# Kernel optimization log

Hardware: AMD Instinct MI355X
Metric: run time of the kernel (lower is better)

## Reference

```python
import jax, jax.numpy as jnp
import numpy as np

B, S, D = 32, 2048, 8
H = 256
COUPLING = -1.0  # TC['WOBBLE_COUPLING'] default
WOBBLE_STEP = 0.03125


def setup_inputs() -> dict:
    key = jax.random.key(0)
    k = jax.random.split(key, 5)
    return {
        'x': jax.random.normal(k[0], (B, S, D), dtype=jnp.float32),
        'We': jax.random.normal(k[1], (H, D), dtype=jnp.float32) * 0.35,
        'be': jax.random.normal(k[2], (H,), dtype=jnp.float32) * 0.02,
        'Wr': jax.random.normal(k[3], (256, 7 * H), dtype=jnp.float32) * 0.02,
        'br': jax.random.normal(k[4], (256,), dtype=jnp.float32) * 0.02,
    }


def _forward(x, We, be, Wr, br):
    Bm, Sm, _ = x.shape
    h = We.shape[0]

    def step(carry, xt):
        ph, wb, prev_xt, has_prev = carry
        pt = xt @ We.T + be                      # [B,h] embedded phase increments
        # xpt = stack([cos(pt), sin(pt)]); accumulator consumes the spinor pair,
        # equivalent to the wrapped phase delta atan2(sin, cos)
        delta = jnp.arctan2(jnp.sin(pt), jnp.cos(pt))
        wb2 = wb + WOBBLE_STEP
        is_rep = has_prev * jnp.all(xt == prev_xt, axis=1, keepdims=True).astype(x.dtype)
        # WobblePhaseAccumulator(spinor=True): phase advances by delta plus
        # coupling-modulated wobble; wobble channel accumulates delta
        ph_out = ph + delta + COUPLING * jnp.sin(wb2)
        wb_out = wb2 + delta
        ph_new = ph_out
        wb_new = is_rep * wb_out + (1.0 - is_rep) * wb2
        ph_s = 0.5 * ph_new
        readout = jnp.concatenate([
            jnp.cos(ph_new), jnp.sin(ph_new),
            jnp.cos(ph_s), jnp.sin(ph_s),
            jnp.cos(wb_new), jnp.sin(wb_new),
            ph_new,
        ], axis=1)                                # [B, 7h]
        logits = readout @ Wr.T + br              # [B, 256]
        return (ph_new, wb_new, xt, jnp.ones((), x.dtype)), (logits, ph_new, wb_new)

    ph0 = jnp.zeros((Bm, h), x.dtype)
    wb0 = jnp.zeros((Bm, h), x.dtype)
    prev0 = jnp.zeros((Bm, x.shape[2]), x.dtype)
    carry0 = (ph0, wb0, prev0, jnp.zeros((), x.dtype))
    xs = jnp.swapaxes(x, 0, 1)                    # [S,B,D]
    _, (logits, ph_hist, wb_hist) = jax.lax.scan(step, carry0, xs)
    logits = jnp.swapaxes(logits, 0, 1)           # [B,S,256]
    ph_hist = jnp.swapaxes(ph_hist, 0, 1)         # [B,S,h]
    wb_hist = jnp.swapaxes(wb_hist, 0, 1)         # [B,S,h]
    return logits, ph_hist, wb_hist


def reference(x, We, be, Wr, br):
    return _forward(x, We, be, Wr, br)
```

## Files before the change

kernel.cpp:

```cpp
#include <hip/hip_runtime.h>
#include <hip/hip_bf16.h>
#include <math.h>

#define NB 32
#define NS 2048
#define ND 8
#define NH 256
#define NK 1792
#define NO 256
#define NM (NB*NS)
#define WSTEP 0.03125f
#define CCH 64
#define LCH (NS/CCH)

typedef __attribute__((ext_vector_type(8))) short short8;
typedef __attribute__((ext_vector_type(4))) float f32x4;

__device__ float g_ssum[NB*CCH*NH];
__device__ float g_wb0 [NB*CCH*NH];
__device__ float g_esum[NB*CCH*NH];
__device__ float g_ph0 [NB*CCH*NH];
__device__ float g_rep [NB*NS];

__device__ __forceinline__ float fast_sin(float x){
    float r = x * 0.15915494309189535f;
    r = r - floorf(r);
    return __builtin_amdgcn_sinf(r);
}
__device__ __forceinline__ float fast_cos(float x){
    float r = x * 0.15915494309189535f;
    r = r - floorf(r);
    return __builtin_amdgcn_cosf(r);
}
__device__ __forceinline__ unsigned short bf16_rn(float f){
    union { float f; unsigned int u; } v; v.f = f;
    unsigned int u = v.u;
    unsigned int r = (u + 0x7FFFu + ((u >> 16) & 1u)) >> 16;
    return (unsigned short)r;
}
__device__ __forceinline__ float xform(int c, float v){
    switch(c){
        case 0: case 4: return fast_cos(v);
        case 1: case 5: return fast_sin(v);
        case 2:         return fast_cos(0.5f*v);
        case 3:         return fast_sin(0.5f*v);
        default:        return v;
    }
}

extern "C" __global__ __launch_bounds__(256)
void k_delta(const float* __restrict__ x, const float* __restrict__ We,
             const float* __restrict__ be, float* __restrict__ delta){
    int blk = blockIdx.x;
    int b = blk >> 6;
    int c = blk & (CCH-1);
    int t0 = c * LCH;
    int h = threadIdx.x;
    __shared__ float xs[(LCH+1)*ND];
    __shared__ float rep[LCH];

    for(int i = h; i < (LCH+1)*ND/4; i += 256){
        int row  = i >> 1;
        int col4 = (i & 1) * 4;
        int t = t0 - 1 + row; if(t < 0) t = 0;
        *(float4*)&xs[row*ND + col4] = *(const float4*)&x[((size_t)b*NS + t)*ND + col4];
    }
    __syncthreads();
    if(h < LCH){
        int t = t0 + h;
        float fl = 0.f;
        if(t > 0){
            bool eq = true;
            #pragma unroll
            for(int d2 = 0; d2 < ND; ++d2) eq = eq && (xs[(h+1)*ND+d2] == xs[h*ND+d2]);
            fl = eq ? 1.f : 0.f;
        }
        rep[h] = fl;
        g_rep[b*NS + t] = fl;
    }
    __syncthreads();

    float4 w0 = *(const float4*)&We[h*ND];
    float4 w1 = *(const float4*)&We[h*ND + 4];
    float bh = be[h];
    float ssum = 0.f;
    for(int j = 0; j < LCH; ++j){
        const float* xr = &xs[(j+1)*ND];
        float pt = bh + xr[0]*w0.x + xr[1]*w0.y + xr[2]*w0.z + xr[3]*w0.w
                      + xr[4]*w1.x + xr[5]*w1.y + xr[6]*w1.z + xr[7]*w1.w;
        float s, cc;
        sincosf(pt, &s, &cc);
        float d = atan2f(s, cc);
        delta[((size_t)(t0+j)*NB + b)*NH + h] = d;
        ssum += WSTEP + rep[j]*d;
    }
    g_ssum[(b*CCH + c)*NH + h] = ssum;
}

extern "C" __global__ __launch_bounds__(256)
void k_prefix_s(){
    int g = blockIdx.x*256 + threadIdx.x;
    int b = g >> 8, h = g & 255;
    float acc = 0.f;
    for(int c = 0; c < CCH; ++c){
        size_t idx = ((size_t)(b*CCH + c))*NH + h;
        g_wb0[idx] = acc;
        acc += g_ssum[idx];
    }
}
extern "C" __global__ __launch_bounds__(256)
void k_prefix_e(){
    int g = blockIdx.x*256 + threadIdx.x;
    int b = g >> 8, h = g & 255;
    float acc = 0.f;
    for(int c = 0; c < CCH; ++c){
        size_t idx = ((size_t)(b*CCH + c))*NH + h;
        g_ph0[idx] = acc;
        acc += g_esum[idx];
    }
}

extern "C" __global__ __launch_bounds__(256)
void k_escan(const float* __restrict__ delta, float* __restrict__ wb_hist){
    int blk = blockIdx.x;
    int b = blk >> 6, c = blk & (CCH-1), t0 = c*LCH, h = threadIdx.x;
    __shared__ float rep[LCH];
    if(h < LCH) rep[h] = g_rep[b*NS + t0 + h];
    __syncthreads();
    float wb = g_wb0[(b*CCH + c)*NH + h];
    const float* dp = delta + (size_t)t0*NB*NH + b*NH + h;
    float* wp = wb_hist + ((size_t)b*NS + t0)*NH + h;
    float d[LCH];
    #pragma unroll
    for(int j = 0; j < LCH; ++j) d[j] = dp[(size_t)j*(NB*NH)];
    float esum = 0.f;
    #pragma unroll
    for(int j = 0; j < LCH; ++j){
        float wb2 = wb + WSTEP;
        float e = d[j] - sinf(wb2);
        esum += e;
        wb = wb2 + rep[j]*d[j];
        wp[(size_t)j*NH] = wb;
    }
    g_esum[(b*CCH + c)*NH + h] = esum;
}

extern "C" __global__ __launch_bounds__(256)
void k_phw(const float* __restrict__ delta, float* __restrict__ ph_hist){
    int blk = blockIdx.x;
    int b = blk >> 6, c = blk & (CCH-1), t0 = c*LCH, h = threadIdx.x;
    __shared__ float rep[LCH];
    if(h < LCH) rep[h] = g_rep[b*NS + t0 + h];
    __syncthreads();
    float wb = g_wb0[(b*CCH + c)*NH + h];
    float ph = g_ph0[(b*CCH + c)*NH + h];
    const float* dp = delta + (size_t)t0*NB*NH + b*NH + h;
    float* pp = ph_hist + ((size_t)b*NS + t0)*NH + h;
    float d[LCH];
    #pragma unroll
    for(int j = 0; j < LCH; ++j) d[j] = dp[(size_t)j*(NB*NH)];
    #pragma unroll
    for(int j = 0; j < LCH; ++j){
        float wb2 = wb + WSTEP;
        float e = d[j] - sinf(wb2);
        ph += e;
        wb = wb2 + rep[j]*d[j];
        pp[(size_t)j*NH] = ph;
    }
}

extern "C" __global__ __launch_bounds__(512)
void k_logits(const float* __restrict__ ph_hist, const float* __restrict__ wb_hist,
              const float* __restrict__ Wr, const float* __restrict__ br,
              float* __restrict__ logits){
    __shared__ __align__(16) unsigned short Al[128][40];
    __shared__ __align__(16) unsigned short Bl[256][40];
    int tid  = threadIdx.x;
    int m0   = blockIdx.x * 128;
    int lane = tid & 63, wid = tid >> 6;
    int wm = wid >> 2, wn = wid & 3;

    f32x4 acc[4][4];
    f32x4 zz = {0.f, 0.f, 0.f, 0.f};
    #pragma unroll
    for(int i = 0; i < 4; ++i)
        #pragma unroll
        for(int j = 0; j < 4; ++j) acc[i][j] = zz;

    int arow = tid >> 2, ah = (tid & 3) * 8;
    int bn   = tid >> 1, bk = (tid & 1) * 16;

    for(int ks = 0; ks < NK/32; ++ks){
        int k0 = ks * 32;
        int c  = k0 >> 8;
        int hb = k0 & 255;

        {
            const float* src = (c == 4 || c == 5) ? wb_hist : ph_hist;
            const float* p = src + (size_t)(m0 + arow)*NH + hb + ah;
            float4 v0 = *(const float4*)p;
            float4 v1 = *(const float4*)(p + 4);
            float v[8] = {v0.x, v0.y, v0.z, v0.w, v1.x, v1.y, v1.z, v1.w};
            unsigned int pk[4];
            #pragma unroll
            for(int j = 0; j < 4; ++j){
                float a0 = xform(c, v[2*j]);
                float a1 = xform(c, v[2*j+1]);
                pk[j] = (unsigned int)bf16_rn(a0) | ((unsigned int)bf16_rn(a1) << 16);
            }
            *(uint4*)&Al[arow][ah] = make_uint4(pk[0], pk[1], pk[2], pk[3]);
        }
        {
            const float* q = Wr + (size_t)bn*NK + k0 + bk;
            float4 q0 = *(const float4*)q;
            float4 q1 = *(const float4*)(q + 4);
            float4 q2 = *(const float4*)(q + 8);
            float4 q3 = *(const float4*)(q + 12);
            float w[16] = {q0.x,q0.y,q0.z,q0.w, q1.x,q1.y,q1.z,q1.w,
                           q2.x,q2.y,q2.z,q2.w, q3.x,q3.y,q3.z,q3.w};
            unsigned int pk[8];
            #pragma unroll
            for(int j = 0; j < 8; ++j)
                pk[j] = (unsigned int)bf16_rn(w[2*j]) | ((unsigned int)bf16_rn(w[2*j+1]) << 16);
            *(uint4*)&Bl[bn][bk]     = make_uint4(pk[0], pk[1], pk[2], pk[3]);
            *(uint4*)&Bl[bn][bk + 8] = make_uint4(pk[4], pk[5], pk[6], pk[7]);
        }
        __syncthreads();

        int kg = lane >> 4, l15 = lane & 15;
        short8 afr[4], bfr[4];
        #pragma unroll
        for(int mf = 0; mf < 4; ++mf)
            afr[mf] = *(const short8*)&Al[wm*64 + mf*16 + l15][kg*8];
        #pragma unroll
        for(int nf = 0; nf < 4; ++nf)
            bfr[nf] = *(const short8*)&Bl[wn*64 + nf*16 + l15][kg*8];
        #pragma unroll
        for(int mf = 0; mf < 4; ++mf)
            #pragma unroll
            for(int nf = 0; nf < 4; ++nf)
                acc[mf][nf] = __builtin_amdgcn_mfma_f32_16x16x32_bf16(
                    afr[mf], bfr[nf], acc[mf][nf], 0, 0, 0);
        __syncthreads();
    }

    int l15 = lane & 15, lg = lane >> 4;
    #pragma unroll
    for(int nf = 0; nf < 4; ++nf){
        int col = wn*64 + nf*16 + l15;
        float bias = br[col];
        #pragma unroll
        for(int mf = 0; mf < 4; ++mf){
            int row = m0 + wm*64 + mf*16 + lg*4;
            #pragma unroll
            for(int r = 0; r < 4; ++r)
                logits[(size_t)(row + r)*NO + col] = acc[mf][nf][r] + bias;
        }
    }
}

extern "C" void kernel_launch(void* const* d_in, const int* in_sizes, int n_in,
                              void* d_out, int out_size, void* d_ws, size_t ws_size,
                              hipStream_t stream){
    const float* x  = (const float*)d_in[0];
    const float* We = (const float*)d_in[1];
    const float* be = (const float*)d_in[2];
    const float* Wr = (const float*)d_in[3];
    const float* br = (const float*)d_in[4];

    float* logits = (float*)d_out;
    float* ph     = logits + (size_t)NM*NO;
    float* wb     = ph + (size_t)NM*NH;
    float* delta  = logits;

    hipLaunchKernelGGL(k_delta,    dim3(NB*CCH), dim3(256), 0, stream, x, We, be, delta);
    hipLaunchKernelGGL(k_prefix_s, dim3(32),     dim3(256), 0, stream);
    hipLaunchKernelGGL(k_escan,    dim3(NB*CCH), dim3(256), 0, stream, delta, wb);
    hipLaunchKernelGGL(k_prefix_e, dim3(32),     dim3(256), 0, stream);
    hipLaunchKernelGGL(k_phw,      dim3(NB*CCH), dim3(256), 0, stream, delta, ph);
    hipLaunchKernelGGL(k_logits,   dim3(NM/128), dim3(512), 0, stream, ph, wb, Wr, br, logits);
}
```

Baseline: 425.1 us.

## Restructure logits GEMM: pre-convert Wr to bf16, register-direct A with shared trig

```diff
diff --git a/kernel.cpp b/kernel.cpp
--- a/kernel.cpp
+++ b/kernel.cpp
@@ -21,31 +21,13 @@
 __device__ float g_esum[NB*CCH*NH];
 __device__ float g_ph0 [NB*CCH*NH];
 __device__ float g_rep [NB*NS];
-
-__device__ __forceinline__ float fast_sin(float x){
-    float r = x * 0.15915494309189535f;
-    r = r - floorf(r);
-    return __builtin_amdgcn_sinf(r);
-}
-__device__ __forceinline__ float fast_cos(float x){
-    float r = x * 0.15915494309189535f;
-    r = r - floorf(r);
-    return __builtin_amdgcn_cosf(r);
-}
+__device__ unsigned short g_bb[NO*NK];
+
 __device__ __forceinline__ unsigned short bf16_rn(float f){
     union { float f; unsigned int u; } v; v.f = f;
     unsigned int u = v.u;
     unsigned int r = (u + 0x7FFFu + ((u >> 16) & 1u)) >> 16;
     return (unsigned short)r;
-}
-__device__ __forceinline__ float xform(int c, float v){
-    switch(c){
-        case 0: case 4: return fast_cos(v);
-        case 1: case 5: return fast_sin(v);
-        case 2:         return fast_cos(0.5f*v);
-        case 3:         return fast_sin(0.5f*v);
-        default:        return v;
-    }
 }
 
 extern "C" __global__ __launch_bounds__(256)
@@ -169,16 +151,53 @@
     }
 }
 
-extern "C" __global__ __launch_bounds__(512)
+extern "C" __global__ __launch_bounds__(256)
+void k_bconv(const float* __restrict__ Wr){
+    int i = (blockIdx.x*256 + threadIdx.x) * 8;
+    if(i >= NO*NK) return;
+    float4 a = *(const float4*)&Wr[i];
+    float4 b = *(const float4*)&Wr[i+4];
+    union { unsigned int u[4]; uint4 v; } r;
+    r.u[0] = (unsigned int)bf16_rn(a.x) | ((unsigned int)bf16_rn(a.y) << 16);
+    r.u[1] = (unsigned int)bf16_rn(a.z) | ((unsigned int)bf16_rn(a.w) << 16);
+    r.u[2] = (unsigned int)bf16_rn(b.x) | ((unsigned int)bf16_rn(b.y) << 16);
+    r.u[3] = (unsigned int)bf16_rn(b.z) | ((unsigned int)bf16_rn(b.w) << 16);
+    *(uint4*)&g_bb[i] = r.v;
+}
+
+#define DO_CH(CH, SRC) do{                                                        \
+    short8 bfr[4];                                                                \
+    _Pragma("unroll")                                                             \
+    for(int nf = 0; nf < 4; ++nf)                                                 \
+        bfr[nf] = *(const short8*)&g_bb[(size_t)(colb + nf*16)*NK + (CH)*256 + hb];\
+    short8 afr[4];                                                                \
+    _Pragma("unroll")                                                             \
+    for(int mf = 0; mf < 4; ++mf){                                                \
+        union{ unsigned int u[4]; short8 s; } r_;                                 \
+        _Pragma("unroll")                                                         \
+        for(int j = 0; j < 4; ++j)                                                \
+            r_.u[j] = (unsigned int)bf16_rn(SRC[mf][2*j])                         \
+                    | ((unsigned int)bf16_rn(SRC[mf][2*j+1]) << 16);              \
+        afr[mf] = r_.s;                                                           \
+    }                                                                             \
+    _Pragma("unroll")                                                             \
+    for(int mf = 0; mf < 4; ++mf)                                                 \
+        _Pragma("unroll")                                                         \
+        for(int nf = 0; nf < 4; ++nf)                                             \
+            acc[mf][nf] = __builtin_amdgcn_mfma_f32_16x16x32_bf16(                \
+                afr[mf], bfr[nf], acc[mf][nf], 0, 0, 0);                          \
+}while(0)
+
+extern "C" __global__ __launch_bounds__(512, 2)
 void k_logits(const float* __restrict__ ph_hist, const float* __restrict__ wb_hist,
-              const float* __restrict__ Wr, const float* __restrict__ br,
-              float* __restrict__ logits){
-    __shared__ __align__(16) unsigned short Al[128][40];
-    __shared__ __align__(16) unsigned short Bl[256][40];
+              const float* __restrict__ br, float* __restrict__ logits){
     int tid  = threadIdx.x;
     int m0   = blockIdx.x * 128;
     int lane = tid & 63, wid = tid >> 6;
     int wm = wid >> 2, wn = wid & 3;
+    int l15 = lane & 15, kg = lane >> 4;
+    int row0 = m0 + wm*64 + l15;
+    int colb = wn*64 + l15;
 
     f32x4 acc[4][4];
     f32x4 zz = {0.f, 0.f, 0.f, 0.f};
@@ -187,64 +206,67 @@
         #pragma unroll
         for(int j = 0; j < 4; ++j) acc[i][j] = zz;
 
-    int arow = tid >> 2, ah = (tid & 3) * 8;
-    int bn   = tid >> 1, bk = (tid & 1) * 16;
-
-    for(int ks = 0; ks < NK/32; ++ks){
-        int k0 = ks * 32;
-        int c  = k0 >> 8;
-        int hb = k0 & 255;
-
-        {
-            const float* src = (c == 4 || c == 5) ? wb_hist : ph_hist;
-            const float* p = src + (size_t)(m0 + arow)*NH + hb + ah;
-            float4 v0 = *(const float4*)p;
-            float4 v1 = *(const float4*)(p + 4);
-            float v[8] = {v0.x, v0.y, v0.z, v0.w, v1.x, v1.y, v1.z, v1.w};
-            unsigned int pk[4];
-            #pragma unroll
-            for(int j = 0; j < 4; ++j){
-                float a0 = xform(c, v[2*j]);
-                float a1 = xform(c, v[2*j+1]);
-                pk[j] = (unsigned int)bf16_rn(a0) | ((unsigned int)bf16_rn(a1) << 16);
+    for(int hc = 0; hc < 8; ++hc){
+        int hb = hc*32 + kg*8;
+        float a0[4][8], s8[4][8], c8[4][8];
+
+        #pragma unroll
+        for(int mf = 0; mf < 4; ++mf){
+            const float* p = ph_hist + (size_t)(row0 + mf*16)*NH + hb;
+            float4 x0 = *(const float4*)p;
+            float4 x1 = *(const float4*)(p + 4);
+            a0[mf][0]=x0.x; a0[mf][1]=x0.y; a0[mf][2]=x0.z; a0[mf][3]=x0.w;
+            a0[mf][4]=x1.x; a0[mf][5]=x1.y; a0[mf][6]=x1.z; a0[mf][7]=x1.w;
+        }
+        DO_CH(6, a0);
+
+        #pragma unroll
+        for(int mf = 0; mf < 4; ++mf)
+            #pragma unroll
+            for(int j = 0; j < 8; ++j){
+                float r = a0[mf][j] * 0.07957747154594767f;
+                r -= floorf(r);
+                s8[mf][j] = __builtin_amdgcn_sinf(r);
+                c8[mf][j] = __builtin_amdgcn_cosf(r);
             }
-            *(uint4*)&Al[arow][ah] = make_uint4(pk[0], pk[1], pk[2], pk[3]);
+        DO_CH(2, c8);
+        DO_CH(3, s8);
+
+        #pragma unroll
+        for(int mf = 0; mf < 4; ++mf)
+            #pragma unroll
+            for(int j = 0; j < 8; ++j)
+                a0[mf][j] = c8[mf][j]*c8[mf][j] - s8[mf][j]*s8[mf][j];
+        DO_CH(0, a0);
+        #pragma unroll
+        for(int mf = 0; mf < 4; ++mf)
+            #pragma unroll
+            for(int j = 0; j < 8; ++j)
+                a0[mf][j] = 2.f * s8[mf][j] * c8[mf][j];
+        DO_CH(1, a0);
+
+        #pragma unroll
+        for(int mf = 0; mf < 4; ++mf){
+            const float* p = wb_hist + (size_t)(row0 + mf*16)*NH + hb;
+            float4 x0 = *(const float4*)p;
+            float4 x1 = *(const float4*)(p + 4);
+            a0[mf][0]=x0.x; a0[mf][1]=x0.y; a0[mf][2]=x0.z; a0[mf][3]=x0.w;
+            a0[mf][4]=x1.x; a0[mf][5]=x1.y; a0[mf][6]=x1.z; a0[mf][7]=x1.w;
         }
-        {
-            const float* q = Wr + (size_t)bn*NK + k0 + bk;
-            float4 q0 = *(const float4*)q;
-            float4 q1 = *(const float4*)(q + 4);
-            float4 q2 = *(const float4*)(q + 8);
-            float4 q3 = *(const float4*)(q + 12);
-            float w[16] = {q0.x,q0.y,q0.z,q0.w, q1.x,q1.y,q1.z,q1.w,
-                           q2.x,q2.y,q2.z,q2.w, q3.x,q3.y,q3.z,q3.w};
-            unsigned int pk[8];
-            #pragma unroll
-            for(int j = 0; j < 8; ++j)
-                pk[j] = (unsigned int)bf16_rn(w[2*j]) | ((unsigned int)bf16_rn(w[2*j+1]) << 16);
-            *(uint4*)&Bl[bn][bk]     = make_uint4(pk[0], pk[1], pk[2], pk[3]);
-            *(uint4*)&Bl[bn][bk + 8] = make_uint4(pk[4], pk[5], pk[6], pk[7]);
-        }
-        __syncthreads();
-
-        int kg = lane >> 4, l15 = lane & 15;
-        short8 afr[4], bfr[4];
         #pragma unroll
         for(int mf = 0; mf < 4; ++mf)
-            afr[mf] = *(const short8*)&Al[wm*64 + mf*16 + l15][kg*8];
-        #pragma unroll
-        for(int nf = 0; nf < 4; ++nf)
-            bfr[nf] = *(const short8*)&Bl[wn*64 + nf*16 + l15][kg*8];
-        #pragma unroll
-        for(int mf = 0; mf < 4; ++mf)
-            #pragma unroll
-            for(int nf = 0; nf < 4; ++nf)
-                acc[mf][nf] = __builtin_amdgcn_mfma_f32_16x16x32_bf16(
-                    afr[mf], bfr[nf], acc[mf][nf], 0, 0, 0);
-        __syncthreads();
-    }
-
-    int l15 = lane & 15, lg = lane >> 4;
+            #pragma unroll
+            for(int j = 0; j < 8; ++j){
+                float r = a0[mf][j] * 0.15915494309189535f;
+                r -= floorf(r);
+                s8[mf][j] = __builtin_amdgcn_sinf(r);
+                c8[mf][j] = __builtin_amdgcn_cosf(r);
+            }
+        DO_CH(4, c8);
+        DO_CH(5, s8);
+    }
+
+    int lg = kg;
     #pragma unroll
     for(int nf = 0; nf < 4; ++nf){
         int col = wn*64 + nf*16 + l15;
@@ -273,10 +295,11 @@
     float* wb     = ph + (size_t)NM*NH;
     float* delta  = logits;
 
+    hipLaunchKernelGGL(k_bconv,    dim3((NO*NK/8 + 255)/256), dim3(256), 0, stream, Wr);
     hipLaunchKernelGGL(k_delta,    dim3(NB*CCH), dim3(256), 0, stream, x, We, be, delta);
     hipLaunchKernelGGL(k_prefix_s, dim3(32),     dim3(256), 0, stream);
     hipLaunchKernelGGL(k_escan,    dim3(NB*CCH), dim3(256), 0, stream, delta, wb);
     hipLaunchKernelGGL(k_prefix_e, dim3(32),     dim3(256), 0, stream);
     hipLaunchKernelGGL(k_phw,      dim3(NB*CCH), dim3(256), 0, stream, delta, ph);
-    hipLaunchKernelGGL(k_logits,   dim3(NM/128), dim3(512), 0, stream, ph, wb, Wr, br, logits);
-}
+    hipLaunchKernelGGL(k_logits,   dim3(NM/128), dim3(512), 0, stream, ph, wb, br, logits);
+}
```

Result: slower. 447.1 us (+5.2%).
